# Performance work log

Hardware: AMD Instinct MI355X
Metric: run time of the kernel (lower is better)

## Reference

```python
import jax, jax.numpy as jnp
import numpy as np

NUM_HEADS = 16  # matches init_kwargs


def _linear(x, W, b):
    # torch nn.Linear: x @ W.T + b
    return jnp.matmul(x, W.T) + b


def setup_inputs() -> dict:
    key = jax.random.key(0)
    ks = jax.random.split(key, 5)
    B, S, Dm = 8, 2048, 1024
    scale = 0.02
    return {
        "q": jax.random.normal(ks[0], (B, S, Dm), dtype=jnp.float32),
        "k": jax.random.normal(ks[1], (B, S, Dm), dtype=jnp.float32),
        "v": jax.random.normal(ks[2], (B, S, Dm), dtype=jnp.float32),
        "W": jax.random.normal(ks[3], (Dm, Dm), dtype=jnp.float32) * scale,
        "b": jax.random.normal(ks[4], (Dm,), dtype=jnp.float32) * scale,
    }


def reference(q, k, v, W, b):
    B, S, Dm = q.shape
    H = NUM_HEADS
    D = Dm // H  # head_dim

    def proj(x):
        # linear -> view(B, S, H, D) -> transpose(2, 3): (B, S, D, H)
        # NOTE: original code transposes dims 2 and 3 (head_dim <-> heads),
        # NOT the usual (1, 2); we reproduce that exactly.
        y = _linear(x, W, b).reshape(B, S, H, D)
        return jnp.swapaxes(y, 2, 3)  # (B, S, D, H)

    qh, kh, vh = proj(q), proj(k), proj(v)

    # scores: (B, S, D, H) @ (B, S, H, D) -> (B, S, D, D), scaled by sqrt(head_dim)
    logits = jnp.einsum("bsdh,bseh->bsde", qh, kh) / jnp.sqrt(jnp.float32(D))
    attn = jax.nn.softmax(logits, axis=-1)
    out = jnp.einsum("bsde,bseh->bsdh", attn, vh)  # (B, S, D, H)

    # transpose(1, 2) -> (B, D, S, H), then view(B, -1, model_dim)
    concat = jnp.swapaxes(out, 1, 2).reshape(B, -1, Dm)  # (B, S, Dm)
    return _linear(concat, W, b)
```

## Files before the change

kernel.cpp:

```cpp
#include <hip/hip_runtime.h>
#include <hip/hip_fp16.h>
#include <math.h>

typedef _Float16 f16;
typedef _Float16 half8_t __attribute__((ext_vector_type(8)));
typedef _Float16 half2_t __attribute__((ext_vector_type(2)));
typedef __fp16   fp16x2  __attribute__((ext_vector_type(2)));
typedef float    float4_t __attribute__((ext_vector_type(4)));

__device__ f16 Wh[1024 * 1024];

__device__ __forceinline__ void gl_lds16(const void* g, void* l) {
    __builtin_amdgcn_global_load_lds(
        (const __attribute__((address_space(1))) void*)g,
        (__attribute__((address_space(3))) void*)l,
        16, 0, 0);
}

__device__ __forceinline__ half2_t pkrtz(float a, float b) {
    fp16x2 r = __builtin_amdgcn_cvt_pkrtz(a, b);
    return __builtin_bit_cast(half2_t, r);
}

__device__ __forceinline__ float fdot2(half2_t a, half2_t b, float c) {
    return __builtin_amdgcn_fdot2(__builtin_bit_cast(fp16x2, a),
                                  __builtin_bit_cast(fp16x2, b), c, false);
}

__device__ __forceinline__ half8_t cvt8(float4_t lo, float4_t hi) {
    half2_t p0 = pkrtz(lo[0], lo[1]);
    half2_t p1 = pkrtz(lo[2], lo[3]);
    half2_t p2 = pkrtz(hi[0], hi[1]);
    half2_t p3 = pkrtz(hi[2], hi[3]);
    half8_t r;
    r[0] = p0[0]; r[1] = p0[1]; r[2] = p1[0]; r[3] = p1[1];
    r[4] = p2[0]; r[5] = p2[1]; r[6] = p3[0]; r[7] = p3[1];
    return r;
}

__global__ __launch_bounds__(256) void convert_w_kernel(const float* __restrict__ W) {
    const int i = (blockIdx.x * 256 + threadIdx.x) * 8;
    const float4_t a = *(const float4_t*)(W + i);
    const float4_t b = *(const float4_t*)(W + i + 4);
    half8_t h;
#pragma unroll
    for (int t = 0; t < 4; ++t) h[t] = (f16)a[t];
#pragma unroll
    for (int t = 0; t < 4; ++t) h[4 + t] = (f16)b[t];
    *(half8_t*)(Wh + i) = h;
}


__device__ __forceinline__ void stage16(const f16* __restrict__ base, f16* dst,
                                        int tid, int kt) {
#pragma unroll
    for (int it = 0; it < 4; ++it) {
        const int ch = tid + it * 512;
        const int r = ch >> 3, s = ch & 7;
        gl_lds16(base + (size_t)r * 1024 + kt + ((s ^ (r & 7)) << 3), dst + ch * 8);
    }
}

__device__ __forceinline__ void loadA32(const float* __restrict__ base, int tid,
                                        int kt, int itbase, float4_t g[4]) {
#pragma unroll
    for (int it = 0; it < 2; ++it) {
        const int ch = tid + (itbase + it) * 512;
        const int r = ch >> 3, s = ch & 7;
        const float* p = base + (size_t)r * 1024 + kt + ((s ^ (r & 7)) << 3);
        g[2 * it]     = *(const float4_t*)p;
        g[2 * it + 1] = *(const float4_t*)(p + 4);
    }
}

__device__ __forceinline__ void writeA32(f16* dst, int tid, int itbase,
                                         const float4_t g[4]) {
#pragma unroll
    for (int it = 0; it < 2; ++it) {
        const int ch = tid + (itbase + it) * 512;
        *(half8_t*)(dst + ch * 8) = cvt8(g[2 * it], g[2 * it + 1]);
    }
}

template <typename TA, typename TC>
__device__ __forceinline__ void gemm_tile256(const TA* __restrict__ A,
                                             const float* __restrict__ bias,
                                             TC* __restrict__ C) {
    constexpr int K = 1024, N = 1024, NT = 16;
    constexpr bool AF32 = (sizeof(TA) == 4);
    __shared__ __align__(16) f16 smem[65536];
    f16* const Asb = smem;
    f16* const Bsb = smem + 32768;

    const int tid  = threadIdx.x;
    const int lane = tid & 63;
    const int wave = tid >> 6;
    const int wr   = wave >> 2;
    const int wc   = wave & 3;
    const int lrow = lane & 15;
    const int kq   = lane >> 4;
    const int row0 = blockIdx.x * 256;
    const int col0 = blockIdx.y * 256;

    const f16*   Ag16 = nullptr;
    const float* Ag32 = nullptr;
    if constexpr (AF32) Ag32 = (const float*)A + (size_t)row0 * K;
    else                Ag16 = (const f16*)A + (size_t)row0 * K;
    const f16* const Bg = Wh + (size_t)col0 * K;

    float4_t acc[8][4];
#pragma unroll
    for (int i = 0; i < 8; ++i)
#pragma unroll
        for (int j = 0; j < 4; ++j)
            acc[i][j] = (float4_t){0.f, 0.f, 0.f, 0.f};

    if constexpr (AF32) {
        stage16(Bg, Bsb, tid, 0);
        float4_t g0[4], g1[4];
        loadA32(Ag32, tid, 0, 0, g0);
        loadA32(Ag32, tid, 0, 2, g1);
        writeA32(Asb, tid, 0, g0);
        writeA32(Asb, tid, 2, g1);
        asm volatile("s_waitcnt vmcnt(0)" ::: "memory");
        asm volatile("s_waitcnt lgkmcnt(0)" ::: "memory");
    } else {
        stage16(Ag16, Asb, tid, 0);
        stage16(Bg, Bsb, tid, 0);
    }

    for (int u = 0; u < NT; ++u) {
        const int cur = u & 1;
        const f16* const Ac = Asb + (cur << 14);
        const f16* const Bc = Bsb + (cur << 14);
        f16* const An = Asb + ((cur ^ 1) << 14);
        f16* const Bn = Bsb + ((cur ^ 1) << 14);
        const int kn = ((u + 1) & (NT - 1)) * 64;

        float4_t ga[4];
        stage16(Bg, Bn, tid, kn);
        if constexpr (AF32) {
            loadA32(Ag32, tid, kn, 0, ga);
        } else {
            stage16(Ag16, An, tid, kn);
        }
        asm volatile("s_waitcnt vmcnt(8)" ::: "memory");
        __builtin_amdgcn_s_barrier();

        half8_t bfv[4][2];
#pragma unroll
        for (int j = 0; j < 4; ++j) {
            const int n = wc * 64 + j * 16 + lrow;
#pragma unroll
            for (int ks = 0; ks < 2; ++ks)
                bfv[j][ks] = *(const half8_t*)(Bc + n * 64 + (((ks * 4 + kq) ^ (n & 7)) << 3));
        }

        {
            half8_t afv[4][2];
#pragma unroll
            for (int i = 0; i < 4; ++i) {
                const int m = wr * 128 + i * 16 + lrow;
#pragma unroll
                for (int ks = 0; ks < 2; ++ks)
                    afv[i][ks] = *(const half8_t*)(Ac + m * 64 + (((ks * 4 + kq) ^ (m & 7)) << 3));
            }
            __builtin_amdgcn_s_setprio(1);
#pragma unroll
            for (int i = 0; i < 4; ++i)
#pragma unroll
                for (int j = 0; j < 4; ++j)
#pragma unroll
                    for (int ks = 0; ks < 2; ++ks)
                        acc[i][j] = __builtin_amdgcn_mfma_f32_16x16x32_f16(
                            afv[i][ks], bfv[j][ks], acc[i][j], 0, 0, 0);
            __builtin_amdgcn_s_setprio(0);
        }

        if constexpr (AF32) {
            writeA32(An, tid, 0, ga);
            loadA32(Ag32, tid, kn, 2, ga);
        }

        {
            half8_t afv[4][2];
#pragma unroll
            for (int i = 0; i < 4; ++i) {
                const int m = wr * 128 + (4 + i) * 16 + lrow;
#pragma unroll
                for (int ks = 0; ks < 2; ++ks)
                    afv[i][ks] = *(const half8_t*)(Ac + m * 64 + (((ks * 4 + kq) ^ (m & 7)) << 3));
            }
            __builtin_amdgcn_s_setprio(1);
#pragma unroll
            for (int i = 0; i < 4; ++i)
#pragma unroll
                for (int j = 0; j < 4; ++j)
#pragma unroll
                    for (int ks = 0; ks < 2; ++ks)
                        acc[4 + i][j] = __builtin_amdgcn_mfma_f32_16x16x32_f16(
                            afv[i][ks], bfv[j][ks], acc[4 + i][j], 0, 0, 0);
            __builtin_amdgcn_s_setprio(0);
        }

        if constexpr (AF32) {
            writeA32(An, tid, 2, ga);
        }
        asm volatile("s_waitcnt lgkmcnt(0)" ::: "memory");
        __builtin_amdgcn_s_barrier();
    }
    asm volatile("s_waitcnt vmcnt(0)" ::: "memory");

    const int ccol  = lane & 15;
    const int rbase = (lane >> 4) << 2;
#pragma unroll
    for (int j = 0; j < 4; ++j) {
        const int gcol = col0 + wc * 64 + j * 16 + ccol;
        const float bv = bias[gcol];
#pragma unroll
        for (int i = 0; i < 8; ++i) {
#pragma unroll
            for (int r = 0; r < 4; ++r) {
                const int grow = row0 + wr * 128 + i * 16 + rbase + r;
                C[(size_t)grow * N + gcol] = (TC)(acc[i][j][r] + bv);
            }
        }
    }
}

template <typename TA, typename TC>
__global__ __launch_bounds__(512, 2) void gemm_kernel(
    const TA* __restrict__ A, const float* __restrict__ bias,
    TC* __restrict__ C) {
    gemm_tile256<TA, TC>(A, bias, C);
}

__global__ __launch_bounds__(512, 2) void gemm_proj_kernel(
    const float* __restrict__ q, const float* __restrict__ k,
    const float* __restrict__ v, const float* __restrict__ bias,
    f16* __restrict__ cq, f16* __restrict__ ck, f16* __restrict__ cv) {
    const int z = blockIdx.z;
    const float* A = (z == 0) ? q : (z == 1) ? k : v;
    f16*         C = (z == 0) ? cq : (z == 1) ? ck : cv;
    gemm_tile256<float, f16>(A, bias, C);
}

__global__ __launch_bounds__(256) void attn_kernel(
    const f16* __restrict__ pq, const f16* __restrict__ pk,
    const f16* __restrict__ pv, f16* __restrict__ outp)
{
    __shared__ __align__(16) f16 Ks[4][64][24];
    __shared__ __align__(16) f16 Vs[4][16][72];
    const int lane = threadIdx.x & 63;
    const int wave = threadIdx.x >> 6;
    const int p = blockIdx.x * 4 + wave;
    const int b = p >> 11;
    const int s = p & 2047;
    const f16* qptr = pq + (size_t)p * 1024;
    const f16* kptr = pk + (size_t)p * 1024;
    const f16* vptr = pv + (size_t)p * 1024;

    {
        const int h  = lane >> 2;
        const int e0 = (lane & 3) << 4;
        const half8_t k0 = *(const half8_t*)(kptr + lane * 16);
        const half8_t k1 = *(const half8_t*)(kptr + lane * 16 + 8);
#pragma unroll
        for (int t = 0; t < 8; ++t) {
            Ks[wave][e0 + t][h]     = k0[t];
            Ks[wave][e0 + 8 + t][h] = k1[t];
        }
        const half8_t v0 = *(const half8_t*)(vptr + lane * 16);
        const half8_t v1 = *(const half8_t*)(vptr + lane * 16 + 8);
        *(half8_t*)&Vs[wave][h][e0]     = v0;
        *(half8_t*)&Vs[wave][h][e0 + 8] = v1;
    }
    half2_t qp2[8];
#pragma unroll
    for (int h2 = 0; h2 < 8; ++h2) {
        half2_t t;
        t[0] = qptr[(2 * h2) * 64 + lane];
        t[1] = qptr[(2 * h2 + 1) * 64 + lane];
        qp2[h2] = t;
    }
    __syncthreads();

    float a[64];
#pragma unroll
    for (int e = 0; e < 64; ++e) {
        const half8_t* kr = (const half8_t*)&Ks[wave][e][0];
        const half8_t ka = kr[0];
        const half8_t kb = kr[1];
        float acc = 0.f;
#pragma unroll
        for (int t = 0; t < 4; ++t) {
            half2_t k2a; k2a[0] = ka[2 * t]; k2a[1] = ka[2 * t + 1];
            half2_t k2b; k2b[0] = kb[2 * t]; k2b[1] = kb[2 * t + 1];
            acc = fdot2(qp2[t], k2a, acc);
            acc = fdot2(qp2[4 + t], k2b, acc);
        }
        a[e] = acc;
    }

    float m = a[0];
#pragma unroll
    for (int e = 1; e < 64; ++e) m = fmaxf(m, a[e]);
    float sum = 0.f;
#pragma unroll
    for (int e = 0; e < 64; ++e) {
        const float t = __expf((a[e] - m) * 0.125f);
        a[e] = t;
        sum += t;
    }
    const float inv = 1.f / sum;

    half2_t pk2[32];
#pragma unroll
    for (int e2 = 0; e2 < 32; ++e2)
        pk2[e2] = pkrtz(a[2 * e2], a[2 * e2 + 1]);

    float o[16];
#pragma unroll
    for (int h = 0; h < 16; ++h) {
        const half8_t* vr = (const half8_t*)&Vs[wave][h][0];
        float acc = 0.f;
#pragma unroll
        for (int q8 = 0; q8 < 8; ++q8) {
            const half8_t vv = vr[q8];
#pragma unroll
            for (int t = 0; t < 4; ++t) {
                half2_t v2; v2[0] = vv[2 * t]; v2[1] = vv[2 * t + 1];
                acc = fdot2(pk2[q8 * 4 + t], v2, acc);
            }
        }
        o[h] = acc;
    }

    half8_t o0, o1;
#pragma unroll
    for (int h = 0; h < 8; ++h) o0[h] = (f16)(o[h] * inv);
#pragma unroll
    for (int h = 0; h < 8; ++h) o1[h] = (f16)(o[8 + h] * inv);
    f16* dst = outp + ((size_t)(b * 64 + lane) * 2048 + s) * 16;
    *(half8_t*)dst       = o0;
    *(half8_t*)(dst + 8) = o1;
}

extern "C" void kernel_launch(void* const* d_in, const int* in_sizes, int n_in,
                              void* d_out, int out_size, void* d_ws, size_t ws_size,
                              hipStream_t stream)
{
    const float* q    = (const float*)d_in[0];
    const float* k    = (const float*)d_in[1];
    const float* v    = (const float*)d_in[2];
    const float* W    = (const float*)d_in[3];
    const float* bias = (const float*)d_in[4];
    float* out = (float*)d_out;

    const int M = 16384;
    const size_t elems = (size_t)M * 1024;

    f16* projq = (f16*)d_ws;
    f16* attn  = projq + elems;
    f16* projk = (f16*)d_out;
    f16* projv = projk + elems;

    convert_w_kernel<<<512, 256, 0, stream>>>(W);

    dim3 gridp(M / 256, 1024 / 256, 3);
    gemm_proj_kernel<<<gridp, 512, 0, stream>>>(q, k, v, bias, projq, projk, projv);
    attn_kernel<<<M / 4, 256, 0, stream>>>(projq, projk, projv, attn);
    dim3 gridf(M / 256, 1024 / 256);
    gemm_kernel<f16, float><<<gridf, 512, 0, stream>>>(attn, bias, out);
}
```

Before: 427.1 us.

## Use MFMA for per-position attention and coalesce output stores via LDS

```diff
diff --git a/kernel.cpp b/kernel.cpp
--- a/kernel.cpp
+++ b/kernel.cpp
@@ -4,6 +4,7 @@
 
 typedef _Float16 f16;
 typedef _Float16 half8_t __attribute__((ext_vector_type(8)));
+typedef _Float16 half4_t __attribute__((ext_vector_type(4)));
 typedef _Float16 half2_t __attribute__((ext_vector_type(2)));
 typedef __fp16   fp16x2  __attribute__((ext_vector_type(2)));
 typedef float    float4_t __attribute__((ext_vector_type(4)));
@@ -20,11 +21,6 @@
 __device__ __forceinline__ half2_t pkrtz(float a, float b) {
     fp16x2 r = __builtin_amdgcn_cvt_pkrtz(a, b);
     return __builtin_bit_cast(half2_t, r);
-}
-
-__device__ __forceinline__ float fdot2(half2_t a, half2_t b, float c) {
-    return __builtin_amdgcn_fdot2(__builtin_bit_cast(fp16x2, a),
-                                  __builtin_bit_cast(fp16x2, b), c, false);
 }
 
 __device__ __forceinline__ half8_t cvt8(float4_t lo, float4_t hi) {
@@ -137,14 +133,17 @@
         f16* const Bn = Bsb + ((cur ^ 1) << 14);
         const int kn = ((u + 1) & (NT - 1)) * 64;
 
-        float4_t ga[4];
-        stage16(Bg, Bn, tid, kn);
+        float4_t ga0[4], ga1[4];
         if constexpr (AF32) {
-            loadA32(Ag32, tid, kn, 0, ga);
+            loadA32(Ag32, tid, kn, 0, ga0);
+            loadA32(Ag32, tid, kn, 2, ga1);
+            stage16(Bg, Bn, tid, kn);
+            asm volatile("s_waitcnt vmcnt(12)" ::: "memory");
         } else {
             stage16(Ag16, An, tid, kn);
-        }
-        asm volatile("s_waitcnt vmcnt(8)" ::: "memory");
+            stage16(Bg, Bn, tid, kn);
+            asm volatile("s_waitcnt vmcnt(8)" ::: "memory");
+        }
         __builtin_amdgcn_s_barrier();
 
         half8_t bfv[4][2];
@@ -178,8 +177,7 @@
         }
 
         if constexpr (AF32) {
-            writeA32(An, tid, 0, ga);
-            loadA32(Ag32, tid, kn, 2, ga);
+            writeA32(An, tid, 0, ga0);
         }
 
         {
@@ -204,7 +202,7 @@
         }
 
         if constexpr (AF32) {
-            writeA32(An, tid, 2, ga);
+            writeA32(An, tid, 2, ga1);
         }
         asm volatile("s_waitcnt lgkmcnt(0)" ::: "memory");
         __builtin_amdgcn_s_barrier();
@@ -249,101 +247,122 @@
     const f16* __restrict__ pq, const f16* __restrict__ pk,
     const f16* __restrict__ pv, f16* __restrict__ outp)
 {
+    __shared__ __align__(16) f16 Qs[4][64][24];
     __shared__ __align__(16) f16 Ks[4][64][24];
     __shared__ __align__(16) f16 Vs[4][16][72];
+    __shared__ __align__(16) f16 Os[4][64][24];
     const int lane = threadIdx.x & 63;
     const int wave = threadIdx.x >> 6;
-    const int p = blockIdx.x * 4 + wave;
-    const int b = p >> 11;
-    const int s = p & 2047;
+    const int p0 = blockIdx.x * 4;
+    const int p = p0 + wave;
     const f16* qptr = pq + (size_t)p * 1024;
     const f16* kptr = pk + (size_t)p * 1024;
     const f16* vptr = pv + (size_t)p * 1024;
 
     {
         const int h  = lane >> 2;
-        const int e0 = (lane & 3) << 4;
+        const int c0 = (lane & 3) << 4;
+        const half8_t q0 = *(const half8_t*)(qptr + lane * 16);
+        const half8_t q1 = *(const half8_t*)(qptr + lane * 16 + 8);
         const half8_t k0 = *(const half8_t*)(kptr + lane * 16);
         const half8_t k1 = *(const half8_t*)(kptr + lane * 16 + 8);
 #pragma unroll
         for (int t = 0; t < 8; ++t) {
-            Ks[wave][e0 + t][h]     = k0[t];
-            Ks[wave][e0 + 8 + t][h] = k1[t];
+            Qs[wave][c0 + t][h]     = q0[t];
+            Qs[wave][c0 + 8 + t][h] = q1[t];
+            Ks[wave][c0 + t][h]     = k0[t];
+            Ks[wave][c0 + 8 + t][h] = k1[t];
         }
         const half8_t v0 = *(const half8_t*)(vptr + lane * 16);
         const half8_t v1 = *(const half8_t*)(vptr + lane * 16 + 8);
-        *(half8_t*)&Vs[wave][h][e0]     = v0;
-        *(half8_t*)&Vs[wave][h][e0 + 8] = v1;
-    }
-    half2_t qp2[8];
-#pragma unroll
-    for (int h2 = 0; h2 < 8; ++h2) {
-        half2_t t;
-        t[0] = qptr[(2 * h2) * 64 + lane];
-        t[1] = qptr[(2 * h2 + 1) * 64 + lane];
-        qp2[h2] = t;
+        *(half8_t*)&Vs[wave][h][c0]     = v0;
+        *(half8_t*)&Vs[wave][h][c0 + 8] = v1;
     }
     __syncthreads();
 
-    float a[64];
-#pragma unroll
-    for (int e = 0; e < 64; ++e) {
-        const half8_t* kr = (const half8_t*)&Ks[wave][e][0];
-        const half8_t ka = kr[0];
-        const half8_t kb = kr[1];
-        float acc = 0.f;
-#pragma unroll
-        for (int t = 0; t < 4; ++t) {
-            half2_t k2a; k2a[0] = ka[2 * t]; k2a[1] = ka[2 * t + 1];
-            half2_t k2b; k2b[0] = kb[2 * t]; k2b[1] = kb[2 * t + 1];
-            acc = fdot2(qp2[t], k2a, acc);
-            acc = fdot2(qp2[4 + t], k2b, acc);
-        }
-        a[e] = acc;
-    }
-
-    float m = a[0];
-#pragma unroll
-    for (int e = 1; e < 64; ++e) m = fmaxf(m, a[e]);
-    float sum = 0.f;
-#pragma unroll
-    for (int e = 0; e < 64; ++e) {
-        const float t = __expf((a[e] - m) * 0.125f);
-        a[e] = t;
-        sum += t;
-    }
-    const float inv = 1.f / sum;
-
-    half2_t pk2[32];
-#pragma unroll
-    for (int e2 = 0; e2 < 32; ++e2)
-        pk2[e2] = pkrtz(a[2 * e2], a[2 * e2 + 1]);
-
-    float o[16];
-#pragma unroll
-    for (int h = 0; h < 16; ++h) {
-        const half8_t* vr = (const half8_t*)&Vs[wave][h][0];
-        float acc = 0.f;
-#pragma unroll
-        for (int q8 = 0; q8 < 8; ++q8) {
-            const half8_t vv = vr[q8];
-#pragma unroll
-            for (int t = 0; t < 4; ++t) {
-                half2_t v2; v2[0] = vv[2 * t]; v2[1] = vv[2 * t + 1];
-                acc = fdot2(pk2[q8 * 4 + t], v2, acc);
+    const int g  = lane >> 4;
+    const int lc = lane & 15;
+
+    half4_t ka[4], qb[4];
+#pragma unroll
+    for (int t = 0; t < 4; ++t) {
+        ka[t] = *(const half4_t*)&Ks[wave][16 * t + lc][4 * g];
+        qb[t] = *(const half4_t*)&Qs[wave][16 * t + lc][4 * g];
+    }
+    float4_t s[4][4];
+#pragma unroll
+    for (int et = 0; et < 4; ++et)
+#pragma unroll
+        for (int dt = 0; dt < 4; ++dt)
+            s[et][dt] = __builtin_amdgcn_mfma_f32_16x16x16f16(
+                ka[et], qb[dt], (float4_t){0.f, 0.f, 0.f, 0.f}, 0, 0, 0);
+
+    float inv[4];
+#pragma unroll
+    for (int dt = 0; dt < 4; ++dt) {
+        float m = s[0][dt][0];
+#pragma unroll
+        for (int et = 0; et < 4; ++et)
+#pragma unroll
+            for (int r = 0; r < 4; ++r) m = fmaxf(m, s[et][dt][r]);
+        m = fmaxf(m, __shfl_xor(m, 16));
+        m = fmaxf(m, __shfl_xor(m, 32));
+        float sum = 0.f;
+#pragma unroll
+        for (int et = 0; et < 4; ++et)
+#pragma unroll
+            for (int r = 0; r < 4; ++r) {
+                const float t = __expf((s[et][dt][r] - m) * 0.125f);
+                s[et][dt][r] = t;
+                sum += t;
             }
-        }
-        o[h] = acc;
-    }
-
-    half8_t o0, o1;
-#pragma unroll
-    for (int h = 0; h < 8; ++h) o0[h] = (f16)(o[h] * inv);
-#pragma unroll
-    for (int h = 0; h < 8; ++h) o1[h] = (f16)(o[8 + h] * inv);
-    f16* dst = outp + ((size_t)(b * 64 + lane) * 2048 + s) * 16;
-    *(half8_t*)dst       = o0;
-    *(half8_t*)(dst + 8) = o1;
+        sum += __shfl_xor(sum, 16);
+        sum += __shfl_xor(sum, 32);
+        inv[dt] = 1.f / sum;
+    }
+
+    half4_t pa[4][4];
+#pragma unroll
+    for (int kt = 0; kt < 4; ++kt)
+#pragma unroll
+        for (int dt = 0; dt < 4; ++dt) {
+            const half2_t lo = pkrtz(s[kt][dt][0] * inv[dt], s[kt][dt][1] * inv[dt]);
+            const half2_t hi = pkrtz(s[kt][dt][2] * inv[dt], s[kt][dt][3] * inv[dt]);
+            half4_t f;
+            f[0] = lo[0]; f[1] = lo[1]; f[2] = hi[0]; f[3] = hi[1];
+            pa[kt][dt] = f;
+        }
+
+    float4_t o[4];
+#pragma unroll
+    for (int dt = 0; dt < 4; ++dt) o[dt] = (float4_t){0.f, 0.f, 0.f, 0.f};
+#pragma unroll
+    for (int kt = 0; kt < 4; ++kt) {
+        const half4_t vb = *(const half4_t*)&Vs[wave][lc][16 * kt + 4 * g];
+#pragma unroll
+        for (int dt = 0; dt < 4; ++dt)
+            o[dt] = __builtin_amdgcn_mfma_f32_16x16x16f16(pa[kt][dt], vb, o[dt], 0, 0, 0);
+    }
+
+#pragma unroll
+    for (int dt = 0; dt < 4; ++dt)
+#pragma unroll
+        for (int r = 0; r < 4; ++r)
+            Os[wave][16 * dt + 4 * g + r][lc] = (f16)o[dt][r];
+    __syncthreads();
+
+    const int b0 = p0 >> 11;
+    const int s0 = p0 & 2047;
+#pragma unroll
+    for (int hf = 0; hf < 2; ++hf) {
+        const int u  = threadIdx.x + hf * 256;
+        const int d  = u >> 3;
+        const int si = (u >> 1) & 3;
+        const int uh = u & 1;
+        const half8_t val = *(const half8_t*)&Os[si][d][uh * 8];
+        f16* dst = outp + ((size_t)(b0 * 64 + d) * 2048 + (s0 + si)) * 16 + uh * 8;
+        *(half8_t*)dst = val;
+    }
 }
 
 extern "C" void kernel_launch(void* const* d_in, const int* in_sizes, int n_in,
```

New measurement: 463.4 us. 8.5% more time.
